# Kernel optimization log

Hardware: AMD Instinct MI355X
Metric: run time of the kernel (lower is better)

## Reference

```python
import jax, jax.numpy as jnp
import numpy as np

LOG_HALF = float(np.log(0.5))  # log_g(0) = log(relu(0)+0.5) = log(0.5)

def log_g(x):
    # log of g(x) = where(x>=0, x+0.5, sigmoid(x))
    return jnp.where(x >= 0.0, jnp.log(jnp.maximum(x, 0.0) + 0.5), -jax.nn.softplus(-x))

def setup_inputs() -> dict:
    key = jax.random.key(0)
    k1, k2, k3, k4 = jax.random.split(key, 4)
    B, T, D, E = 4, 4096, 1024, 1536
    x = jax.random.normal(k1, (B, T, D), dtype=jnp.float32)
    W_f = jax.random.normal(k2, (2 * E, D), dtype=jnp.float32) * 0.02
    b_f = jax.random.normal(k3, (2 * E,), dtype=jnp.float32) * 0.02
    W_down = jax.random.normal(k4, (D, E), dtype=jnp.float32) * 0.02
    return {"x": x, "W_f": W_f, "b_f": b_f, "W_down": W_down}

def reference(x, W_f, b_f, W_down):
    B, T, D = x.shape
    E = W_down.shape[1]
    # fused input projection, split into gate pre-act k and candidate pre-act h_x
    kz, h_x = jnp.split(jnp.einsum('btd,ed->bte', x, W_f) + b_f, 2, axis=-1)
    log_z = -jax.nn.softplus(-kz)          # log sigmoid(k)
    log_coeffs = -jax.nn.softplus(kz)      # log (1 - sigmoid(k))
    log_tilde_h = log_g(h_x)
    # prepend initial log hidden state log_g(0) = log 0.5
    log_h0 = jnp.full((B, 1, E), LOG_HALF, dtype=x.dtype)
    log_values = jnp.concatenate([log_h0, log_tilde_h + log_z], axis=1)  # (B, T+1, E)
    # a_star = pad(cumsum(log_coeffs), one zero row at front along time)
    a_star = jnp.concatenate(
        [jnp.zeros((B, 1, E), dtype=x.dtype), jnp.cumsum(log_coeffs, axis=1)], axis=1)
    log_h = a_star + jax.lax.cumlogsumexp(log_values - a_star, axis=1)
    h = jnp.exp(log_h)[:, 1:]              # (B, T, E)
    return jnp.einsum('bte,de->btd', h, W_down)
```

## Files before the change

kernel.cpp:

```cpp
#include <hip/hip_runtime.h>
#include <hip/hip_bf16.h>
#include <stdint.h>


typedef __bf16 bf16x8 __attribute__((ext_vector_type(8)));
typedef float  f32x4  __attribute__((ext_vector_type(4)));

__device__ __forceinline__ uint16_t f32_to_bf16(float f) {
  union { float f; uint32_t u; } v; v.f = f;
  uint32_t r = (v.u + 0x7FFFu + ((v.u >> 16) & 1u)) >> 16;
  return (uint16_t)r;
}
__device__ __forceinline__ float bf16_to_f32(uint16_t u) {
  union { uint32_t u; float f; } v; v.u = ((uint32_t)u) << 16;
  return v.f;
}

__device__ __forceinline__ void gload_lds16(const uint16_t* g, uint16_t* l) {
  __builtin_amdgcn_global_load_lds(
      (__attribute__((address_space(1))) void*)(g),
      (__attribute__((address_space(3))) void*)(l), 16, 0, 0);
}

__global__ __launch_bounds__(256) void cast_f32_bf16(
    const float* __restrict__ in, uint16_t* __restrict__ out, int n4) {
  int i = blockIdx.x * blockDim.x + threadIdx.x;
  if (i >= n4) return;
  float4 v = reinterpret_cast<const float4*>(in)[i];
  ushort4 o;
  o.x = f32_to_bf16(v.x); o.y = f32_to_bf16(v.y);
  o.z = f32_to_bf16(v.z); o.w = f32_to_bf16(v.w);
  reinterpret_cast<ushort4*>(out)[i] = o;
}

template <int OUT_BF16_BIAS>
__global__ __launch_bounds__(512, 1) void gemm256(
    const uint16_t* __restrict__ A, const uint16_t* __restrict__ Bt,
    const float* __restrict__ bias, void* __restrict__ Cout,
    int M, int N, int K) {
  __shared__ alignas(16) uint16_t lds[4 * 16384];

  const int tid  = threadIdx.x;
  const int wave = tid >> 6;
  const int lane = tid & 63;
  const int wr = wave >> 2;
  const int wc = wave & 3;

  const int l  = (int)blockIdx.x >> 3;
  const int x  = (int)blockIdx.x & 7;
  const int m0 = (x * 8 + (l & 7)) << 8;
  const int n0 = (l >> 3) << 8;

  const int NT = K >> 5;

  const int srow = wave * 16 + (lane >> 2);
  const int skg  = (lane & 3) ^ ((lane >> 3) & 3);
  const uint16_t* Ag0 = A  + (size_t)(m0 + srow) * K + skg * 8;
  const uint16_t* Ag1 = A  + (size_t)(m0 + 128 + srow) * K + skg * 8;
  const uint16_t* Bg0 = Bt + (size_t)(n0 + srow) * K + skg * 8;
  const uint16_t* Bg1 = Bt + (size_t)(n0 + 128 + srow) * K + skg * 8;
  const int sdw = wave * 512;

  const int kgq = (lane >> 4) ^ ((lane >> 1) & 3);
  const int rA = (wr * 128 + (lane & 15)) * 32 + kgq * 8;
  const int rB = (wc * 64  + (lane & 15)) * 32 + kgq * 8;

  f32x4 acc[8][4] = {};

#pragma unroll
  for (int tt = 0; tt < 3; ++tt) {
    uint16_t* sb = &lds[tt * 16384];
    gload_lds16(Ag0 + tt * 32, sb + sdw);
    gload_lds16(Ag1 + tt * 32, sb + 4096 + sdw);
    gload_lds16(Bg0 + tt * 32, sb + 8192 + sdw);
    gload_lds16(Bg1 + tt * 32, sb + 12288 + sdw);
  }

#define PH_BAR_IN()  do { __builtin_amdgcn_s_barrier(); \
                          __builtin_amdgcn_sched_barrier(0); \
                          __builtin_amdgcn_s_setprio(1); } while (0)
#define PH_BAR_OUT() do { __builtin_amdgcn_s_setprio(0); \
                          __builtin_amdgcn_sched_barrier(0); \
                          __builtin_amdgcn_s_barrier(); } while (0)

  for (int u = 0; u < NT; ++u) {
    const uint16_t* Ab = &lds[(u & 3) * 16384 + rA];
    const uint16_t* Bb = &lds[(u & 3) * 16384 + 8192 + rB];
    const int us = (u + 3 < NT) ? (u + 3) : (NT - 1);
    uint16_t* sb = &lds[((u + 3) & 3) * 16384];
    const size_t kofs = (size_t)us * 32;

    asm volatile("s_waitcnt vmcnt(8)" ::: "memory");
    __builtin_amdgcn_s_barrier();

    bf16x8 af[8], bfr[4];
#pragma unroll
    for (int m = 0; m < 4; ++m) af[m] = *reinterpret_cast<const bf16x8*>(Ab + m * 512);
#pragma unroll
    for (int n = 0; n < 2; ++n) bfr[n] = *reinterpret_cast<const bf16x8*>(Bb + n * 512);
    gload_lds16(Ag0 + kofs, sb + sdw);
    PH_BAR_IN();
#pragma unroll
    for (int m = 0; m < 4; ++m)
#pragma unroll
      for (int n = 0; n < 2; ++n)
        acc[m][n] = __builtin_amdgcn_mfma_f32_16x16x32_bf16(bfr[n], af[m], acc[m][n], 0, 0, 0);
    PH_BAR_OUT();

#pragma unroll
    for (int m = 4; m < 8; ++m) af[m] = *reinterpret_cast<const bf16x8*>(Ab + m * 512);
    gload_lds16(Ag1 + kofs, sb + 4096 + sdw);
    PH_BAR_IN();
#pragma unroll
    for (int m = 4; m < 8; ++m)
#pragma unroll
      for (int n = 0; n < 2; ++n)
        acc[m][n] = __builtin_amdgcn_mfma_f32_16x16x32_bf16(bfr[n], af[m], acc[m][n], 0, 0, 0);
    PH_BAR_OUT();

#pragma unroll
    for (int n = 2; n < 4; ++n) bfr[n] = *reinterpret_cast<const bf16x8*>(Bb + n * 512);
    gload_lds16(Bg0 + kofs, sb + 8192 + sdw);
    PH_BAR_IN();
#pragma unroll
    for (int m = 0; m < 4; ++m)
#pragma unroll
      for (int n = 2; n < 4; ++n)
        acc[m][n] = __builtin_amdgcn_mfma_f32_16x16x32_bf16(bfr[n], af[m], acc[m][n], 0, 0, 0);
    PH_BAR_OUT();

    gload_lds16(Bg1 + kofs, sb + 12288 + sdw);
    PH_BAR_IN();
#pragma unroll
    for (int m = 4; m < 8; ++m)
#pragma unroll
      for (int n = 2; n < 4; ++n)
        acc[m][n] = __builtin_amdgcn_mfma_f32_16x16x32_bf16(bfr[n], af[m], acc[m][n], 0, 0, 0);
    __builtin_amdgcn_s_setprio(0);
    __builtin_amdgcn_sched_barrier(0);
  }
  asm volatile("s_waitcnt vmcnt(0)" ::: "memory");

  const int r0 = m0 + wr * 128 + (lane & 15);
  const int cb = n0 + wc * 64 + (lane >> 4) * 4;
  if constexpr (OUT_BF16_BIAS) {
    uint16_t* C = (uint16_t*)Cout;
#pragma unroll
    for (int n = 0; n < 4; ++n) {
      const int col = cb + n * 16;
      const float4 bv = *reinterpret_cast<const float4*>(&bias[col]);
#pragma unroll
      for (int m = 0; m < 8; ++m) {
        const int row = r0 + m * 16;
        ushort4 o;
        o.x = f32_to_bf16(acc[m][n][0] + bv.x);
        o.y = f32_to_bf16(acc[m][n][1] + bv.y);
        o.z = f32_to_bf16(acc[m][n][2] + bv.z);
        o.w = f32_to_bf16(acc[m][n][3] + bv.w);
        *reinterpret_cast<ushort4*>(&C[(size_t)row * N + col]) = o;
      }
    }
  } else {
    float* C = (float*)Cout;
#pragma unroll
    for (int n = 0; n < 4; ++n) {
      const int col = cb + n * 16;
#pragma unroll
      for (int m = 0; m < 8; ++m) {
        const int row = r0 + m * 16;
        float4 o;
        o.x = acc[m][n][0]; o.y = acc[m][n][1];
        o.z = acc[m][n][2]; o.w = acc[m][n][3];
        *reinterpret_cast<float4*>(&C[(size_t)row * N + col]) = o;
      }
    }
  }
#undef PH_BAR_IN
#undef PH_BAR_OUT
}

__device__ __forceinline__ void gate_val(float kz, float hx, float& a, float& v) {
  float ek = __expf(-fabsf(kz));
  float r  = 1.0f / (1.0f + ek);
  float z  = (kz >= 0.0f) ? r : ek * r;
  a        = (kz >= 0.0f) ? ek * r : r;
  float g;
  if (hx >= 0.0f) {
    g = hx + 0.5f;
  } else {
    float eh = __expf(hx);
    g = eh / (1.0f + eh);
  }
  v = z * g;
}

__global__ __launch_bounds__(256) void scan_pass1(
    const uint16_t* __restrict__ proj, float* __restrict__ Ac,
    float* __restrict__ Vc, int T, int E, int CH, int L) {
  const int e = blockIdx.x * 256 + threadIdx.x;
  const int c = blockIdx.y;
  const int b = blockIdx.z;
  const int N1 = 2 * E;
  const uint16_t* p = proj + (size_t)(b * T + c * L) * N1 + e;
  float A = 1.0f, V = 0.0f;
  for (int t = 0; t < L; ++t) {
    float kz = bf16_to_f32(p[0]);
    float hx = bf16_to_f32(p[E]);
    float a, v; gate_val(kz, hx, a, v);
    A *= a;
    V = a * V + v;
    p += N1;
  }
  const size_t idx = ((size_t)(b * CH + c)) * E + e;
  Ac[idx] = A; Vc[idx] = V;
}

__global__ __launch_bounds__(256) void scan_pass2(
    const float* __restrict__ Ac, const float* __restrict__ Vc,
    float* __restrict__ hstart, int E, int CH) {
  const int e = blockIdx.x * 256 + threadIdx.x;
  const int b = blockIdx.y;
  float h = 0.5f;
  for (int c = 0; c < CH; ++c) {
    const size_t idx = ((size_t)(b * CH + c)) * E + e;
    hstart[idx] = h;
    h = Ac[idx] * h + Vc[idx];
  }
}

__global__ __launch_bounds__(256) void scan_pass3(
    const uint16_t* __restrict__ proj, const float* __restrict__ hstart,
    uint16_t* __restrict__ hout, int T, int E, int CH, int L) {
  const int e = blockIdx.x * 256 + threadIdx.x;
  const int c = blockIdx.y;
  const int b = blockIdx.z;
  const int N1 = 2 * E;
  const uint16_t* p = proj + (size_t)(b * T + c * L) * N1 + e;
  uint16_t* o = hout + (size_t)(b * T + c * L) * E + e;
  float h = hstart[((size_t)(b * CH + c)) * E + e];
  for (int t = 0; t < L; ++t) {
    float kz = bf16_to_f32(p[0]);
    float hx = bf16_to_f32(p[E]);
    float a, v; gate_val(kz, hx, a, v);
    h = a * h + v;
    *o = f32_to_bf16(h);
    p += N1; o += E;
  }
}

extern "C" void kernel_launch(void* const* d_in, const int* in_sizes, int n_in,
                              void* d_out, int out_size, void* d_ws, size_t ws_size,
                              hipStream_t stream) {
  const float* x   = (const float*)d_in[0];
  const float* W_f = (const float*)d_in[1];
  const float* b_f = (const float*)d_in[2];
  const float* W_d = (const float*)d_in[3];
  const int Bb = 4, T = 4096, D = 1024, E = 1536;
  const int M = Bb * T;
  const int N1 = 2 * E;
  const int CH = 64, L = T / CH;

  char* w = (char*)d_ws;
  uint16_t* x_bf  = (uint16_t*)w; w += (size_t)M * D * 2;
  uint16_t* Wf_bf = (uint16_t*)w; w += (size_t)N1 * D * 2;
  uint16_t* Wd_bf = (uint16_t*)w; w += (size_t)D * E * 2;
  uint16_t* proj  = (uint16_t*)w; w += (size_t)M * N1 * 2;
  uint16_t* h_bf  = (uint16_t*)w; w += (size_t)M * E * 2;
  float* Ac     = (float*)w; w += (size_t)Bb * CH * E * 4;
  float* Vc     = (float*)w; w += (size_t)Bb * CH * E * 4;
  float* hstart = (float*)w; w += (size_t)Bb * CH * E * 4;

  cast_f32_bf16<<<M * D / 4 / 256, 256, 0, stream>>>(x, x_bf, M * D / 4);
  cast_f32_bf16<<<N1 * D / 4 / 256, 256, 0, stream>>>(W_f, Wf_bf, N1 * D / 4);
  cast_f32_bf16<<<D * E / 4 / 256, 256, 0, stream>>>(W_d, Wd_bf, D * E / 4);

  gemm256<1><<<(M / 256) * (N1 / 256), 512, 0, stream>>>(
      x_bf, Wf_bf, b_f, proj, M, N1, D);

  scan_pass1<<<dim3(E / 256, CH, Bb), 256, 0, stream>>>(proj, Ac, Vc, T, E, CH, L);
  scan_pass2<<<dim3(E / 256, Bb), 256, 0, stream>>>(Ac, Vc, hstart, E, CH);
  scan_pass3<<<dim3(E / 256, CH, Bb), 256, 0, stream>>>(proj, hstart, h_bf, T, E, CH, L);

  gemm256<0><<<(M / 256) * (D / 256), 512, 0, stream>>>(
      h_bf, Wd_bf, nullptr, d_out, M, D, E);
}
```

Measured before the change: 290.0 us.

## Drop per-phase barriers in GEMM loop and allow two blocks per CU

Replaces the four-phase ping-pong schedule, which placed workgroup barriers around each MFMA quarter, with one barrier per K-step. All four async global-to-LDS loads are issued up front, then two MFMA halves run, with the second half's A fragments loaded from LDS in between. Launch bounds change from one to two blocks per CU so a second workgroup can hide latency. The risk is that the register limit implied by two 512-thread blocks (32 f32x4 accumulators plus fragments) forces spills. The 128 KB LDS buffer may also prevent a second block from fitting at all.

```diff
diff --git a/kernel.cpp b/kernel.cpp
--- a/kernel.cpp
+++ b/kernel.cpp
@@ -34,7 +34,7 @@
 }
 
 template <int OUT_BF16_BIAS>
-__global__ __launch_bounds__(512, 1) void gemm256(
+__global__ __launch_bounds__(512, 2) void gemm256(
     const uint16_t* __restrict__ A, const uint16_t* __restrict__ Bt,
     const float* __restrict__ bias, void* __restrict__ Cout,
     int M, int N, int K) {
@@ -76,13 +76,6 @@
     gload_lds16(Bg1 + tt * 32, sb + 12288 + sdw);
   }
 
-#define PH_BAR_IN()  do { __builtin_amdgcn_s_barrier(); \
-                          __builtin_amdgcn_sched_barrier(0); \
-                          __builtin_amdgcn_s_setprio(1); } while (0)
-#define PH_BAR_OUT() do { __builtin_amdgcn_s_setprio(0); \
-                          __builtin_amdgcn_sched_barrier(0); \
-                          __builtin_amdgcn_s_barrier(); } while (0)
-
   for (int u = 0; u < NT; ++u) {
     const uint16_t* Ab = &lds[(u & 3) * 16384 + rA];
     const uint16_t* Bb = &lds[(u & 3) * 16384 + 8192 + rB];
@@ -93,49 +86,32 @@
     asm volatile("s_waitcnt vmcnt(8)" ::: "memory");
     __builtin_amdgcn_s_barrier();
 
-    bf16x8 af[8], bfr[4];
-#pragma unroll
-    for (int m = 0; m < 4; ++m) af[m] = *reinterpret_cast<const bf16x8*>(Ab + m * 512);
-#pragma unroll
-    for (int n = 0; n < 2; ++n) bfr[n] = *reinterpret_cast<const bf16x8*>(Bb + n * 512);
+    bf16x8 af0[4], af1[4], bfr[4];
+#pragma unroll
+    for (int m = 0; m < 4; ++m) af0[m] = *reinterpret_cast<const bf16x8*>(Ab + m * 512);
+#pragma unroll
+    for (int n = 0; n < 4; ++n) bfr[n] = *reinterpret_cast<const bf16x8*>(Bb + n * 512);
     gload_lds16(Ag0 + kofs, sb + sdw);
-    PH_BAR_IN();
+    gload_lds16(Ag1 + kofs, sb + 4096 + sdw);
+    gload_lds16(Bg0 + kofs, sb + 8192 + sdw);
+    gload_lds16(Bg1 + kofs, sb + 12288 + sdw);
+    __builtin_amdgcn_sched_barrier(0);
+    __builtin_amdgcn_s_setprio(1);
 #pragma unroll
     for (int m = 0; m < 4; ++m)
 #pragma unroll
-      for (int n = 0; n < 2; ++n)
-        acc[m][n] = __builtin_amdgcn_mfma_f32_16x16x32_bf16(bfr[n], af[m], acc[m][n], 0, 0, 0);
-    PH_BAR_OUT();
-
-#pragma unroll
-    for (int m = 4; m < 8; ++m) af[m] = *reinterpret_cast<const bf16x8*>(Ab + m * 512);
-    gload_lds16(Ag1 + kofs, sb + 4096 + sdw);
-    PH_BAR_IN();
-#pragma unroll
-    for (int m = 4; m < 8; ++m)
-#pragma unroll
-      for (int n = 0; n < 2; ++n)
-        acc[m][n] = __builtin_amdgcn_mfma_f32_16x16x32_bf16(bfr[n], af[m], acc[m][n], 0, 0, 0);
-    PH_BAR_OUT();
-
-#pragma unroll
-    for (int n = 2; n < 4; ++n) bfr[n] = *reinterpret_cast<const bf16x8*>(Bb + n * 512);
-    gload_lds16(Bg0 + kofs, sb + 8192 + sdw);
-    PH_BAR_IN();
+      for (int n = 0; n < 4; ++n)
+        acc[m][n] = __builtin_amdgcn_mfma_f32_16x16x32_bf16(bfr[n], af0[m], acc[m][n], 0, 0, 0);
+    __builtin_amdgcn_s_setprio(0);
+#pragma unroll
+    for (int m = 0; m < 4; ++m) af1[m] = *reinterpret_cast<const bf16x8*>(Ab + (m + 4) * 512);
+    __builtin_amdgcn_sched_barrier(0);
+    __builtin_amdgcn_s_setprio(1);
 #pragma unroll
     for (int m = 0; m < 4; ++m)
 #pragma unroll
-      for (int n = 2; n < 4; ++n)
-        acc[m][n] = __builtin_amdgcn_mfma_f32_16x16x32_bf16(bfr[n], af[m], acc[m][n], 0, 0, 0);
-    PH_BAR_OUT();
-
-    gload_lds16(Bg1 + kofs, sb + 12288 + sdw);
-    PH_BAR_IN();
-#pragma unroll
-    for (int m = 4; m < 8; ++m)
-#pragma unroll
-      for (int n = 2; n < 4; ++n)
-        acc[m][n] = __builtin_amdgcn_mfma_f32_16x16x32_bf16(bfr[n], af[m], acc[m][n], 0, 0, 0);
+      for (int n = 0; n < 4; ++n)
+        acc[m + 4][n] = __builtin_amdgcn_mfma_f32_16x16x32_bf16(bfr[n], af1[m], acc[m + 4][n], 0, 0, 0);
     __builtin_amdgcn_s_setprio(0);
     __builtin_amdgcn_sched_barrier(0);
   }
@@ -175,8 +151,6 @@
       }
     }
   }
-#undef PH_BAR_IN
-#undef PH_BAR_OUT
 }
 
 __device__ __forceinline__ void gate_val(float kz, float hx, float& a, float& v) {
```

Result: no change. 294.0 us (+1.4%).
